# Optimization experiments

Measured on AMD Instinct MI355X. Metric: run time of the kernel, lower is better.

Reference implementation:

```python
import jax, jax.numpy as jnp
import numpy as np

EMB = 768
HEADS = 8
HEAD_DIM = EMB // HEADS  # 96
B, N = 4, 2048


def setup_inputs() -> dict:
    key = jax.random.key(0)
    ks = jax.random.split(key, 9)
    s = 1.0 / np.sqrt(EMB)
    x = jax.random.normal(ks[0], (B, N, EMB), dtype=jnp.float32)
    Wq = jax.random.uniform(ks[1], (EMB, EMB), jnp.float32, -s, s)
    bq = jax.random.uniform(ks[2], (EMB,), jnp.float32, -s, s)
    Wk = jax.random.uniform(ks[3], (EMB, EMB), jnp.float32, -s, s)
    bk = jax.random.uniform(ks[4], (EMB,), jnp.float32, -s, s)
    Wv = jax.random.uniform(ks[5], (EMB, EMB), jnp.float32, -s, s)
    bv = jax.random.uniform(ks[6], (EMB,), jnp.float32, -s, s)
    Wo = jax.random.uniform(ks[7], (EMB, EMB), jnp.float32, -s, s)
    bo = jax.random.uniform(ks[8], (EMB,), jnp.float32, -s, s)
    return {"x": x, "Wq": Wq, "bq": bq, "Wk": Wk, "bk": bk,
            "Wv": Wv, "bv": bv, "Wo": Wo, "bo": bo}


def _split_heads(t):
    b, n, _ = t.shape
    return t.reshape(b, n, HEADS, HEAD_DIM).transpose(0, 2, 1, 3)  # b h n d


def reference(x, Wq, bq, Wk, bk, Wv, bv, Wo, bo):
    q = _split_heads(x @ Wq + bq)
    k = _split_heads(x @ Wk + bk)
    v = _split_heads(x @ Wv + bv)
    # NOTE: faithful to source — softmax on UNSCALED logits, then divide by sqrt(head_dim)
    energy = jnp.einsum('bhqd,bhkd->bhqk', q, k)
    att = jax.nn.softmax(energy, axis=-1) / np.sqrt(HEAD_DIM)
    out = jnp.einsum('bhqk,bhkd->bhqd', att, v)
    out = out.transpose(0, 2, 1, 3).reshape(x.shape[0], x.shape[1], EMB)
    return out @ Wo + bo
```

## Files before the change

### kernel.cpp

```cpp
#include <hip/hip_runtime.h>

typedef _Float16 half_t;
typedef __attribute__((ext_vector_type(8))) _Float16 half8;
typedef __attribute__((ext_vector_type(2))) __fp16 fp16x2;
typedef __attribute__((ext_vector_type(4))) float f32x4;
typedef __attribute__((ext_vector_type(16))) float f32x16;

#define EMB 768
#define HEADS 8
#define HD 96
#define BB 4
#define NN 2048
#define BN (BB*NN)

static __device__ __forceinline__ f32x4 mfma16(half8 a, half8 b, f32x4 c) {
    return __builtin_amdgcn_mfma_f32_16x16x32_f16(a, b, c, 0, 0, 0);
}
static __device__ __forceinline__ f32x16 mfma32(half8 a, half8 b, f32x16 c) {
    return __builtin_amdgcn_mfma_f32_32x32x16_f16(a, b, c, 0, 0, 0);
}
static __device__ __forceinline__ unsigned pkrtz(float a, float b) {
    fp16x2 h = __builtin_amdgcn_cvt_pkrtz(a, b);
    return __builtin_bit_cast(unsigned, h);
}
static __device__ __forceinline__ unsigned sx32(unsigned v) {
    return (unsigned)__shfl_xor((int)v, 32);
}
static __device__ __forceinline__ float max3f(float a, float b, float c) {
    return fmaxf(fmaxf(a, b), c);
}
static __device__ __forceinline__ half8 pack8(float4 a, float4 b) {
    union { unsigned u[4]; half8 h; } t;
    t.u[0] = pkrtz(a.x, a.y); t.u[1] = pkrtz(a.z, a.w);
    t.u[2] = pkrtz(b.x, b.y); t.u[3] = pkrtz(b.z, b.w);
    return t.h;
}

__global__ __launch_bounds__(256) void cvt_transpose_w(
    const float* __restrict__ W0, const float* __restrict__ W1,
    const float* __restrict__ W2, const float* __restrict__ W3,
    half_t* __restrict__ T0, half_t* __restrict__ T1,
    half_t* __restrict__ T2, half_t* __restrict__ T3)
{
    const float* W; half_t* T;
    switch (blockIdx.z) {
        case 0: W = W0; T = T0; break;
        case 1: W = W1; T = T1; break;
        case 2: W = W2; T = T2; break;
        default: W = W3; T = T3; break;
    }
    __shared__ float ls[32][33];
    const int k0 = blockIdx.x * 32, n0 = blockIdx.y * 32;
    const int r = threadIdx.x >> 3, c4 = (threadIdx.x & 7) * 4;
    float4 v = *(const float4*)&W[(size_t)(k0 + r) * EMB + n0 + c4];
    ls[r][c4+0] = v.x; ls[r][c4+1] = v.y; ls[r][c4+2] = v.z; ls[r][c4+3] = v.w;
    __syncthreads();
    union { half_t h[4]; uint2 u; } t;
    #pragma unroll
    for (int j = 0; j < 4; ++j) t.h[j] = (half_t)ls[c4 + j][r];
    *(uint2*)&T[(size_t)(n0 + r) * EMB + k0 + c4] = t.u;
}

__global__ __launch_bounds__(256) void proj_qkv_h(
    const float* __restrict__ x,
    const half_t* __restrict__ WqT, const float* __restrict__ bq,
    const half_t* __restrict__ WkT, const float* __restrict__ bk,
    const half_t* __restrict__ WvT, const float* __restrict__ bv,
    half_t* __restrict__ Qo, half_t* __restrict__ Ko, half_t* __restrict__ Vt)
{
    const half_t* WT; const float* bias;
    const int z = blockIdx.z;
    if (z == 0)      { WT = WqT; bias = bq; }
    else if (z == 1) { WT = WkT; bias = bk; }
    else             { WT = WvT; bias = bv; }

    __shared__ half_t As[128][56];
    __shared__ half_t Bs[128][56];

    const int tid = threadIdx.x;
    const int lane = tid & 63;
    const int wid = tid >> 6;
    const int lr = lane & 15;
    const int lkg = lane >> 4;
    const int wm = (wid >> 1) * 64;
    const int wn = (wid & 1) * 64;
    const int mbase = blockIdx.x * 128;
    const int nbase = blockIdx.y * 128;

    const int srr = tid >> 2;
    const int skk = (tid & 3) * 8;

    f32x4 acc[4][4];
    const f32x4 z4 = {0.f, 0.f, 0.f, 0.f};
    #pragma unroll
    for (int i = 0; i < 4; ++i)
        #pragma unroll
        for (int j = 0; j < 4; ++j) acc[i][j] = z4;

    const float*  aptr = x  + (size_t)(mbase + srr) * EMB + skk;
    const half_t* bptr = WT + (size_t)(nbase + srr) * EMB + skk;

    half8 a0 = pack8(*(const float4*)(aptr),
                     *(const float4*)(aptr + 4));
    half8 a1 = pack8(*(const float4*)(aptr + 64 * EMB),
                     *(const float4*)(aptr + 64 * EMB + 4));
    half8 b0 = *(const half8*)bptr;
    half8 b1 = *(const half8*)(bptr + 64 * EMB);

    for (int k0 = 0; k0 < EMB; k0 += 32) {
        __syncthreads();
        *(half8*)&As[srr][skk]      = a0;
        *(half8*)&As[srr + 64][skk] = a1;
        *(half8*)&Bs[srr][skk]      = b0;
        *(half8*)&Bs[srr + 64][skk] = b1;
        __syncthreads();
        if (k0 + 32 < EMB) {
            a0 = pack8(*(const float4*)(aptr + k0 + 32),
                       *(const float4*)(aptr + k0 + 36));
            a1 = pack8(*(const float4*)(aptr + k0 + 32 + 64 * EMB),
                       *(const float4*)(aptr + k0 + 36 + 64 * EMB));
            b0 = *(const half8*)(bptr + k0 + 32);
            b1 = *(const half8*)(bptr + k0 + 32 + 64 * EMB);
        }
        half8 af[4], bf[4];
        #pragma unroll
        for (int mi = 0; mi < 4; ++mi)
            af[mi] = *(const half8*)&As[wm + mi*16 + lr][lkg*8];
        #pragma unroll
        for (int ni = 0; ni < 4; ++ni)
            bf[ni] = *(const half8*)&Bs[wn + ni*16 + lr][lkg*8];
        #pragma unroll
        for (int mi = 0; mi < 4; ++mi)
            #pragma unroll
            for (int ni = 0; ni < 4; ++ni)
                acc[mi][ni] = mfma16(af[mi], bf[ni], acc[mi][ni]);
    }

    const float qscale = (z == 0) ? 1.4426950408889634f : 1.0f;

    #pragma unroll
    for (int ni = 0; ni < 4; ++ni) {
        const int e = nbase + wn + ni*16 + lr;
        const float be = bias[e];
        const int h = e / HD, d = e % HD;
        #pragma unroll
        for (int mi = 0; mi < 4; ++mi) {
            const int row0 = mbase + wm + mi*16 + lkg*4;
            const int b = row0 >> 11, n0 = row0 & (NN - 1);
            if (z == 2) {
                union { half_t hh[4]; uint2 u; } t;
                #pragma unroll
                for (int r = 0; r < 4; ++r) t.hh[r] = (half_t)(acc[mi][ni][r] + be);
                *(uint2*)&Vt[((size_t)(b*HEADS + h) * HD + d) * NN + n0] = t.u;
            } else {
                half_t* outp = (z == 0) ? Qo : Ko;
                #pragma unroll
                for (int r = 0; r < 4; ++r)
                    outp[((size_t)(b*HEADS + h) * NN + n0 + r) * HD + d] =
                        (half_t)((acc[mi][ni][r] + be) * qscale);
            }
        }
    }
}

__global__ __launch_bounds__(256, 3) void attn_h(
    const half_t* __restrict__ Qh, const half_t* __restrict__ Kh,
    const half_t* __restrict__ Vth, half_t* __restrict__ AOh)
{
    __shared__ __align__(16) char smem[49152];

    const int tid = threadIdx.x;
    const int lane = tid & 63;
    const int wid = tid >> 6;
    const int l31 = lane & 31;
    const int b5 = lane >> 5;
    const int qsub = wid & 1;
    const int sub = wid >> 1;

    const int f = blockIdx.x;
    const int bh = (f & 7) + 8 * (f >> 8);
    const int qbase = ((f >> 3) & 31) * 64;

    const half_t* Qp = Qh + (size_t)bh * NN * HD;
    const half_t* Kp = Kh + (size_t)bh * NN * HD;
    const half_t* Vp = Vth + (size_t)bh * HD * NN;
    half_t* AOp = AOh + (size_t)bh * NN * HD;

    const int kr = tid >> 2;
    const int kcb = (tid & 3) * 48;
    const int vd = tid >> 1;
    const int vcb = (tid & 1) * 64;

    half8 kva, kvb, kvc, vv0, vv1, vv2, vv3;

#define KGLOAD(KT) {                                                          \
        const half_t* ksrc_ = Kp + (size_t)((KT) * 64 + kr) * HD + kcb / 2;   \
        kva = *(const half8*)(ksrc_);                                         \
        kvb = *(const half8*)(ksrc_ + 8);                                     \
        kvc = *(const half8*)(ksrc_ + 16); }
#define VGLOAD(KT) if (tid < 192) {                                           \
        const half_t* vsrc_ = Vp + (size_t)vd * NN + (KT) * 64 + vcb / 2;     \
        vv0 = *(const half8*)(vsrc_);      vv1 = *(const half8*)(vsrc_ + 8);  \
        vv2 = *(const half8*)(vsrc_ + 16); vv3 = *(const half8*)(vsrc_ + 24); }
#define WRITEBUF(BASE) {                                                      \
        char* kb_ = (BASE);                                                   \
        *(half8*)(kb_ + ((kr * 192 + kcb +  0) ^ ((kr & 7) << 4))) = kva;     \
        *(half8*)(kb_ + ((kr * 192 + kcb + 16) ^ ((kr & 7) << 4))) = kvb;     \
        *(half8*)(kb_ + ((kr * 192 + kcb + 32) ^ ((kr & 7) << 4))) = kvc;     \
        if (tid < 192) {                                                      \
            char* vb_ = (BASE) + 12288;                                       \
            *(half8*)(vb_ + ((vd * 128 + vcb +  0) ^ ((vd & 7) << 4))) = vv0; \
            *(half8*)(vb_ + ((vd * 128 + vcb + 16) ^ ((vd & 7) << 4))) = vv1; \
            *(half8*)(vb_ + ((vd * 128 + vcb + 32) ^ ((vd & 7) << 4))) = vv2; \
            *(half8*)(vb_ + ((vd * 128 + vcb + 48) ^ ((vd & 7) << 4))) = vv3; \
        } }

    KGLOAD(0);
    VGLOAD(0);

    {
        const int r = tid >> 2;
        const int cb = (tid & 3) * 48;
        const half_t* src = Qp + (size_t)(qbase + r) * HD + cb / 2;
        #pragma unroll
        for (int c = 0; c < 3; ++c) {
            half8 q = *(const half8*)(src + c * 8);
            *(half8*)(smem + ((r * 192 + cb + c * 16) ^ ((r & 7) << 4))) = q;
        }
    }
    __syncthreads();
    half8 qf[6];
    {
        const int r = qsub * 32 + l31;
        #pragma unroll
        for (int kg = 0; kg < 6; ++kg)
            qf[kg] = *(const half8*)(smem + ((r * 192 + kg * 32 + 16 * b5) ^ ((r & 7) << 4)));
    }
    __syncthreads();

    WRITEBUF(smem);

    f32x16 acc[3];
    const f32x16 z16 = {0.f,0.f,0.f,0.f,0.f,0.f,0.f,0.f,0.f,0.f,0.f,0.f,0.f,0.f,0.f,0.f};
    acc[0] = z16; acc[1] = z16; acc[2] = z16;
    float mreg = -1e30f, lreg = 0.f;

    const int kvrow = sub * 32 + l31;

    for (int kt = 0; kt < NN / 64; ++kt) {
        __syncthreads();

        if (kt + 1 < NN / 64) {
            KGLOAD(kt + 1);
            VGLOAD(kt + 1);
        }

        const char* kb = smem + (kt & 1) * 24576;
        const char* vb = kb + 12288;

        f32x16 st = z16;
        __builtin_amdgcn_s_setprio(1);
        #pragma unroll
        for (int kg = 0; kg < 6; ++kg) {
            half8 kf = *(const half8*)(kb +
                ((kvrow * 192 + kg * 32 + 16 * b5) ^ ((kvrow & 7) << 4)));
            st = mfma32(kf, qf[kg], st);
        }
        __builtin_amdgcn_s_setprio(0);

        float t0 = max3f(st[0],  st[1],  st[2]);
        float t1 = max3f(st[3],  st[4],  st[5]);
        float t2 = max3f(st[6],  st[7],  st[8]);
        float t3 = max3f(st[9],  st[10], st[11]);
        float t4 = max3f(st[12], st[13], st[14]);
        float tm = max3f(max3f(t0, t1, t2), max3f(t3, t4, st[15]),
                         __shfl_xor(max3f(max3f(t0, t1, t2), t3, st[15]), 32));
        {
            float tml = max3f(max3f(t0, t1, t2), max3f(t3, t4, st[15]), -1e30f);
            tm = fmaxf(tml, __shfl_xor(tml, 32));
        }

        if (!__all(tm <= mreg + 8.0f)) {
            const float mn = fmaxf(mreg, tm);
            const float sc = exp2f(mreg - mn);
            lreg *= sc;
            #pragma unroll
            for (int db = 0; db < 3; ++db)
                #pragma unroll
                for (int i = 0; i < 16; ++i) acc[db][i] *= sc;
            mreg = mn;
        }

        float rs = 0.f;
        #pragma unroll
        for (int i = 0; i < 16; ++i) {
            const float p = exp2f(st[i] - mreg);
            st[i] = p;
            rs += p;
        }
        rs += __shfl_xor(rs, 32);
        lreg += rs;

        unsigned pk[4][2];
        #pragma unroll
        for (int rr = 0; rr < 4; ++rr) {
            pk[rr][0] = pkrtz(st[rr*4+0], st[rr*4+1]);
            pk[rr][1] = pkrtz(st[rr*4+2], st[rr*4+3]);
        }

        #pragma unroll
        for (int ks = 0; ks < 2; ++ks) {
            const unsigned z0 = b5 ? pk[2*ks][0] : pk[2*ks+1][0];
            const unsigned z1 = b5 ? pk[2*ks][1] : pk[2*ks+1][1];
            const unsigned x0 = sx32(z0);
            const unsigned x1 = sx32(z1);
            union { unsigned u[4]; half8 h; } afu;
            afu.u[0] = b5 ? x0 : pk[2*ks][0];
            afu.u[1] = b5 ? x1 : pk[2*ks][1];
            afu.u[2] = b5 ? pk[2*ks+1][0] : x0;
            afu.u[3] = b5 ? pk[2*ks+1][1] : x1;
            const half8 af = afu.h;
            __builtin_amdgcn_s_setprio(1);
            #pragma unroll
            for (int db = 0; db < 3; ++db) {
                const int d = db * 32 + l31;
                half8 vf = *(const half8*)(vb +
                    ((d * 128 + sub * 64 + ks * 32 + 16 * b5) ^ ((d & 7) << 4)));
                acc[db] = mfma32(vf, af, acc[db]);
            }
            __builtin_amdgcn_s_setprio(0);
        }

        if (kt + 1 < NN / 64) {
            WRITEBUF(smem + ((kt + 1) & 1) * 24576);
        }
    }

#undef KGLOAD
#undef VGLOAD
#undef WRITEBUF

    float* fb = (float*)smem;
    fb[tid] = mreg;
    fb[256 + tid] = lreg;
    __syncthreads();
    const float mp = fb[tid ^ 128];
    const float lp = fb[256 + (tid ^ 128)];
    const float mc = fmaxf(mreg, mp);
    const float sc = exp2f(mreg - mc);
    const float lc = lreg * sc + lp * exp2f(mp - mc);
    __syncthreads();
    if (wid >= 2) {
        float* rec = fb + (qsub * 64 + lane) * 49;
        #pragma unroll
        for (int db = 0; db < 3; ++db)
            #pragma unroll
            for (int i = 0; i < 16; ++i) rec[db*16 + i] = acc[db][i] * sc;
    }
    __syncthreads();
    if (wid < 2) {
        const float* rec = fb + (qsub * 64 + lane) * 49;
        const float isq = 0.10206207261596577f;
        const float inv = isq / lc;
        const int q = qbase + qsub * 32 + l31;
        half_t* dst = AOp + (size_t)q * HD;
        #pragma unroll
        for (int db = 0; db < 3; ++db)
            #pragma unroll
            for (int rr = 0; rr < 4; ++rr) {
                const int d0 = db * 32 + rr * 8 + 4 * b5;
                union { half_t h[4]; uint2 u; } t;
                #pragma unroll
                for (int r = 0; r < 4; ++r)
                    t.h[r] = (half_t)((acc[db][rr*4 + r] * sc + rec[db*16 + rr*4 + r]) * inv);
                *(uint2*)&dst[d0] = t.u;
            }
    }
}

__global__ __launch_bounds__(256) void proj_out_h(
    const half_t* __restrict__ AOh, const half_t* __restrict__ WoT,
    const float* __restrict__ bo, float* __restrict__ out)
{
    __shared__ half_t As[128][56];
    __shared__ half_t Bs[128][56];

    const int tid = threadIdx.x;
    const int lane = tid & 63;
    const int wid = tid >> 6;
    const int lr = lane & 15;
    const int lkg = lane >> 4;
    const int wm = (wid >> 1) * 64;
    const int wn = (wid & 1) * 64;
    const int mbase = blockIdx.x * 128;
    const int nbase = blockIdx.y * 128;

    const int srr = tid >> 2;
    const int skk = (tid & 3) * 8;

    const int arow0 = mbase + srr;
    const int ab0 = arow0 >> 11, an0 = arow0 & (NN - 1);
    const int arow1 = arow0 + 64;
    const int ab1 = arow1 >> 11, an1 = arow1 & (NN - 1);

    f32x4 acc[4][4];
    const f32x4 z4 = {0.f, 0.f, 0.f, 0.f};
    #pragma unroll
    for (int i = 0; i < 4; ++i)
        #pragma unroll
        for (int j = 0; j < 4; ++j) acc[i][j] = z4;

    const half_t* bptr = WoT + (size_t)(nbase + srr) * EMB + skk;

#define ALOAD(b_, n_, k0_) \
    (*(const half8*)&AOh[((size_t)((b_)*HEADS + (k0_)/HD) * NN + (n_)) * HD + ((k0_)%HD) + skk])

    half8 a0 = ALOAD(ab0, an0, 0);
    half8 a1 = ALOAD(ab1, an1, 0);
    half8 b0 = *(const half8*)bptr;
    half8 b1 = *(const half8*)(bptr + 64 * EMB);

    for (int k0 = 0; k0 < EMB; k0 += 32) {
        __syncthreads();
        *(half8*)&As[srr][skk]      = a0;
        *(half8*)&As[srr + 64][skk] = a1;
        *(half8*)&Bs[srr][skk]      = b0;
        *(half8*)&Bs[srr + 64][skk] = b1;
        __syncthreads();
        if (k0 + 32 < EMB) {
            const int kn = k0 + 32;
            a0 = ALOAD(ab0, an0, kn);
            a1 = ALOAD(ab1, an1, kn);
            b0 = *(const half8*)(bptr + kn);
            b1 = *(const half8*)(bptr + kn + 64 * EMB);
        }
        half8 af[4], bf[4];
        #pragma unroll
        for (int mi = 0; mi < 4; ++mi)
            af[mi] = *(const half8*)&As[wm + mi*16 + lr][lkg*8];
        #pragma unroll
        for (int ni = 0; ni < 4; ++ni)
            bf[ni] = *(const half8*)&Bs[wn + ni*16 + lr][lkg*8];
        #pragma unroll
        for (int mi = 0; mi < 4; ++mi)
            #pragma unroll
            for (int ni = 0; ni < 4; ++ni)
                acc[mi][ni] = mfma16(af[mi], bf[ni], acc[mi][ni]);
    }
#undef ALOAD

    #pragma unroll
    for (int ni = 0; ni < 4; ++ni) {
        const int e = nbase + wn + ni*16 + lr;
        const float be = bo[e];
        #pragma unroll
        for (int mi = 0; mi < 4; ++mi) {
            const int row0 = mbase + wm + mi*16 + lkg*4;
            #pragma unroll
            for (int r = 0; r < 4; ++r)
                out[(size_t)(row0 + r) * EMB + e] = acc[mi][ni][r] + be;
        }
    }
}

extern "C" void kernel_launch(void* const* d_in, const int* in_sizes, int n_in,
                              void* d_out, int out_size, void* d_ws, size_t ws_size,
                              hipStream_t stream)
{
    const float* x  = (const float*)d_in[0];
    const float* Wq = (const float*)d_in[1];
    const float* bq = (const float*)d_in[2];
    const float* Wk = (const float*)d_in[3];
    const float* bk = (const float*)d_in[4];
    const float* Wv = (const float*)d_in[5];
    const float* bv = (const float*)d_in[6];
    const float* Wo = (const float*)d_in[7];
    const float* bo = (const float*)d_in[8];

    const size_t SZ = (size_t)BN * EMB;
    const size_t WS = (size_t)EMB * EMB;

    half_t* ws  = (half_t*)d_ws;
    half_t* WqT = ws;
    half_t* WkT = WqT + WS;
    half_t* WvT = WkT + WS;
    half_t* WoT = WvT + WS;
    half_t* Qh  = WoT + WS;
    half_t* Kh  = Qh  + SZ;
    half_t* Vth = Kh  + SZ;
    half_t* AOh = Vth + SZ;

    cvt_transpose_w<<<dim3(EMB/32, EMB/32, 4), 256, 0, stream>>>(
        Wq, Wk, Wv, Wo, WqT, WkT, WvT, WoT);

    proj_qkv_h<<<dim3(BN/128, EMB/128, 3), 256, 0, stream>>>(
        x, WqT, bq, WkT, bk, WvT, bv, Qh, Kh, Vth);

    attn_h<<<dim3((NN/64) * (BB*HEADS)), 256, 0, stream>>>(Qh, Kh, Vth, AOh);

    proj_out_h<<<dim3(BN/128, EMB/128), 256, 0, stream>>>(AOh, WoT, bo, (float*)d_out);
}
```

Before: 168.5 us.

## Replace double-buffered K/V LDS tiles with a single swizzled buffer

Drops the ping-pong K/V shared-memory buffers in favour of one buffer, written at the top of each iteration and followed by a trailing barrier. Rows now use a 256-byte pitch with a 16-row XOR swizzle. Shared memory per block shrinks from 48 KB to 40 KB, which could let more blocks fit per CU. The cost is an extra __syncthreads per tile and the loss of overlap between LDS writes for the next tile and compute on the current one. Redundant row-max shuffle code is also removed.

After: 167.8 us. No clear change (-0.4%).

```diff
diff --git a/kernel.cpp b/kernel.cpp
--- a/kernel.cpp
+++ b/kernel.cpp
@@ -167,7 +167,7 @@
     const half_t* __restrict__ Qh, const half_t* __restrict__ Kh,
     const half_t* __restrict__ Vth, half_t* __restrict__ AOh)
 {
-    __shared__ __align__(16) char smem[49152];
+    __shared__ __align__(16) char smem[40960];
 
     const int tid = threadIdx.x;
     const int lane = tid & 63;
@@ -202,17 +202,17 @@
         const half_t* vsrc_ = Vp + (size_t)vd * NN + (KT) * 64 + vcb / 2;     \
         vv0 = *(const half8*)(vsrc_);      vv1 = *(const half8*)(vsrc_ + 8);  \
         vv2 = *(const half8*)(vsrc_ + 16); vv3 = *(const half8*)(vsrc_ + 24); }
-#define WRITEBUF(BASE) {                                                      \
-        char* kb_ = (BASE);                                                   \
-        *(half8*)(kb_ + ((kr * 192 + kcb +  0) ^ ((kr & 7) << 4))) = kva;     \
-        *(half8*)(kb_ + ((kr * 192 + kcb + 16) ^ ((kr & 7) << 4))) = kvb;     \
-        *(half8*)(kb_ + ((kr * 192 + kcb + 32) ^ ((kr & 7) << 4))) = kvc;     \
+#define WRITEBUF() {                                                          \
+        char* kb_ = smem;                                                     \
+        *(half8*)(kb_ + ((kr * 256 + kcb +  0) ^ ((kr & 15) << 4))) = kva;    \
+        *(half8*)(kb_ + ((kr * 256 + kcb + 16) ^ ((kr & 15) << 4))) = kvb;    \
+        *(half8*)(kb_ + ((kr * 256 + kcb + 32) ^ ((kr & 15) << 4))) = kvc;    \
         if (tid < 192) {                                                      \
-            char* vb_ = (BASE) + 12288;                                       \
-            *(half8*)(vb_ + ((vd * 128 + vcb +  0) ^ ((vd & 7) << 4))) = vv0; \
-            *(half8*)(vb_ + ((vd * 128 + vcb + 16) ^ ((vd & 7) << 4))) = vv1; \
-            *(half8*)(vb_ + ((vd * 128 + vcb + 32) ^ ((vd & 7) << 4))) = vv2; \
-            *(half8*)(vb_ + ((vd * 128 + vcb + 48) ^ ((vd & 7) << 4))) = vv3; \
+            char* vb_ = smem + 16384;                                         \
+            *(half8*)(vb_ + ((vd * 256 + vcb +  0) ^ ((vd & 15) << 4))) = vv0;\
+            *(half8*)(vb_ + ((vd * 256 + vcb + 16) ^ ((vd & 15) << 4))) = vv1;\
+            *(half8*)(vb_ + ((vd * 256 + vcb + 32) ^ ((vd & 15) << 4))) = vv2;\
+            *(half8*)(vb_ + ((vd * 256 + vcb + 48) ^ ((vd & 15) << 4))) = vv3;\
         } }
 
     KGLOAD(0);
@@ -225,7 +225,7 @@
         #pragma unroll
         for (int c = 0; c < 3; ++c) {
             half8 q = *(const half8*)(src + c * 8);
-            *(half8*)(smem + ((r * 192 + cb + c * 16) ^ ((r & 7) << 4))) = q;
+            *(half8*)(smem + ((r * 256 + cb + c * 16) ^ ((r & 15) << 4))) = q;
         }
     }
     __syncthreads();
@@ -234,11 +234,9 @@
         const int r = qsub * 32 + l31;
         #pragma unroll
         for (int kg = 0; kg < 6; ++kg)
-            qf[kg] = *(const half8*)(smem + ((r * 192 + kg * 32 + 16 * b5) ^ ((r & 7) << 4)));
-    }
-    __syncthreads();
-
-    WRITEBUF(smem);
+            qf[kg] = *(const half8*)(smem + ((r * 256 + kg * 32 + 16 * b5) ^ ((r & 15) << 4)));
+    }
+    __syncthreads();
 
     f32x16 acc[3];
     const f32x16 z16 = {0.f,0.f,0.f,0.f,0.f,0.f,0.f,0.f,0.f,0.f,0.f,0.f,0.f,0.f,0.f,0.f};
@@ -248,6 +246,7 @@
     const int kvrow = sub * 32 + l31;
 
     for (int kt = 0; kt < NN / 64; ++kt) {
+        WRITEBUF();
         __syncthreads();
 
         if (kt + 1 < NN / 64) {
@@ -255,30 +254,23 @@
             VGLOAD(kt + 1);
         }
 
-        const char* kb = smem + (kt & 1) * 24576;
-        const char* vb = kb + 12288;
-
         f32x16 st = z16;
         __builtin_amdgcn_s_setprio(1);
         #pragma unroll
         for (int kg = 0; kg < 6; ++kg) {
-            half8 kf = *(const half8*)(kb +
-                ((kvrow * 192 + kg * 32 + 16 * b5) ^ ((kvrow & 7) << 4)));
+            half8 kf = *(const half8*)(smem +
+                ((kvrow * 256 + kg * 32 + 16 * b5) ^ ((kvrow & 15) << 4)));
             st = mfma32(kf, qf[kg], st);
         }
         __builtin_amdgcn_s_setprio(0);
 
-        float t0 = max3f(st[0],  st[1],  st[2]);
-        float t1 = max3f(st[3],  st[4],  st[5]);
-        float t2 = max3f(st[6],  st[7],  st[8]);
-        float t3 = max3f(st[9],  st[10], st[11]);
-        float t4 = max3f(st[12], st[13], st[14]);
-        float tm = max3f(max3f(t0, t1, t2), max3f(t3, t4, st[15]),
-                         __shfl_xor(max3f(max3f(t0, t1, t2), t3, st[15]), 32));
-        {
-            float tml = max3f(max3f(t0, t1, t2), max3f(t3, t4, st[15]), -1e30f);
-            tm = fmaxf(tml, __shfl_xor(tml, 32));
-        }
+        const float t0 = max3f(st[0],  st[1],  st[2]);
+        const float t1 = max3f(st[3],  st[4],  st[5]);
+        const float t2 = max3f(st[6],  st[7],  st[8]);
+        const float t3 = max3f(st[9],  st[10], st[11]);
+        const float t4 = max3f(st[12], st[13], st[14]);
+        const float tml = fmaxf(max3f(t0, t1, t2), max3f(t3, t4, st[15]));
+        const float tm = fmaxf(tml, __shfl_xor(tml, 32));
 
         if (!__all(tm <= mreg + 8.0f)) {
             const float mn = fmaxf(mreg, tm);
@@ -324,16 +316,13 @@
             #pragma unroll
             for (int db = 0; db < 3; ++db) {
                 const int d = db * 32 + l31;
-                half8 vf = *(const half8*)(vb +
-                    ((d * 128 + sub * 64 + ks * 32 + 16 * b5) ^ ((d & 7) << 4)));
+                half8 vf = *(const half8*)(smem + 16384 +
+                    ((d * 256 + sub * 64 + ks * 32 + 16 * b5) ^ ((d & 15) << 4)));
                 acc[db] = mfma32(vf, af, acc[db]);
             }
             __builtin_amdgcn_s_setprio(0);
         }
-
-        if (kt + 1 < NN / 64) {
-            WRITEBUF(smem + ((kt + 1) & 1) * 24576);
-        }
+        __syncthreads();
     }
 
 #undef KGLOAD
```
